# Optimization experiments

Hardware: AMD Instinct MI355X
Metric: run time of the kernel (lower is better)

## Reference

```python
import jax, jax.numpy as jnp
import numpy as np

N, E = 50000, 800000
IN_C, OUT_C, HEADS = 128, 16, 8
EDGE_DIM = 1
NEG_SLOPE = 0.2
LN_EPS = 1e-5


def setup_inputs() -> dict:
    key = jax.random.key(0)
    ks = jax.random.split(key, 12)
    s = 1.0 / np.sqrt(IN_C)
    HC = OUT_C * HEADS
    return {
        "x": jax.random.normal(ks[0], (N, IN_C), jnp.float32),
        "edge_index": jax.random.randint(ks[1], (2, E), 0, N, jnp.int32),
        "edge_attr": jax.random.normal(ks[2], (E, EDGE_DIM), jnp.float32),
        "W": jax.random.normal(ks[3], (IN_C, HC), jnp.float32) * s,
        "b": jnp.zeros((HC,), jnp.float32),
        "att_src": jax.random.normal(ks[4], (HEADS, OUT_C), jnp.float32) * s,
        "att_dst": jax.random.normal(ks[5], (HEADS, OUT_C), jnp.float32) * s,
        "att_edge": jax.random.normal(ks[6], (HEADS, OUT_C), jnp.float32) * s,
        "lin_edge_w": jax.random.normal(ks[7], (EDGE_DIM, HC), jnp.float32) * s,
        "lin_edge_b": jnp.zeros((HC,), jnp.float32),
        "gamma": jnp.ones((HC,), jnp.float32),
        "beta": jnp.zeros((HC,), jnp.float32),
    }


def _segment_softmax(logits, seg, num_segments):
    # numerically-stable softmax over edges grouped by destination node
    m = jax.ops.segment_max(logits, seg, num_segments=num_segments)
    ex = jnp.exp(logits - m[seg])
    z = jax.ops.segment_sum(ex, seg, num_segments=num_segments)
    return ex / (z[seg] + 1e-16)


def reference(x, edge_index, edge_attr, W, b, att_src, att_dst, att_edge,
              lin_edge_w, lin_edge_b, gamma, beta):
    n = x.shape[0]
    src, dst = edge_index[0], edge_index[1]
    # GAT conv: per-head transform, edge-indexed attention, segment softmax, scatter-add
    h = (x @ W).reshape(n, HEADS, OUT_C)                      # [N,H,C]
    a_src = jnp.einsum('nhc,hc->nh', h, att_src)              # [N,H]
    a_dst = jnp.einsum('nhc,hc->nh', h, att_dst)
    e = (edge_attr @ lin_edge_w + lin_edge_b).reshape(-1, HEADS, OUT_C)
    a_edge = jnp.einsum('ehc,hc->eh', e, att_edge)            # [E,H]
    logits = jax.nn.leaky_relu(a_src[src] + a_dst[dst] + a_edge, NEG_SLOPE)
    alpha = _segment_softmax(logits, dst, n)                  # [E,H]
    msg = alpha[..., None] * h[src]                           # [E,H,C]
    out = jax.ops.segment_sum(msg, dst, num_segments=n).reshape(n, -1) + b
    # residual (in_channels == heads*out_channels -> identity projection)
    out = out + x
    # LayerNorm + ELU (dropout is eval-mode identity)
    mu = jnp.mean(out, axis=-1, keepdims=True)
    var = jnp.var(out, axis=-1, keepdims=True)
    out = (out - mu) * jax.lax.rsqrt(var + LN_EPS) * gamma + beta
    return jax.nn.elu(out)
```

## Files before the change

kernel.cpp:

```cpp
#include <hip/hip_runtime.h>
#include <hip/hip_bf16.h>

#define N_NODES 50000
#define N_EDGES 800000
#define IN_C 128
#define HC 128
#define HEADS 8
#define NEG_SLOPE 0.2f
#define LN_EPS 1e-5f

#define LDH 136
#define ELL_CAP 64
#define GEMM_BLOCKS 782
#define FILL_BLOCKS 782
#define FUSED_BLOCKS (GEMM_BLOCKS + FILL_BLOCKS)

typedef __hip_bfloat16 bf16;
typedef __attribute__((ext_vector_type(8))) short short8;
typedef __attribute__((ext_vector_type(4))) float f32x4;

__device__ __forceinline__ float b2f(bf16 v) { return __bfloat162float(v); }

__device__ __forceinline__ unsigned short f2bf(float f) {
    unsigned u = __float_as_uint(f);
    return (unsigned short)((u + 0x7fffu + ((u >> 16) & 1u)) >> 16);
}
__device__ __forceinline__ float bf2f(unsigned s) {
    return __uint_as_float(s << 16);
}
__device__ __forceinline__ short8 pack8(float4 u, float4 v) {
    short8 r;
    r[0] = (short)f2bf(u.x); r[1] = (short)f2bf(u.y);
    r[2] = (short)f2bf(u.z); r[3] = (short)f2bf(u.w);
    r[4] = (short)f2bf(v.x); r[5] = (short)f2bf(v.y);
    r[6] = (short)f2bf(v.z); r[7] = (short)f2bf(v.w);
    return r;
}

__global__ __launch_bounds__(256) void prep(
    const float* __restrict__ W, unsigned short* __restrict__ Wt,
    int* __restrict__ cnt)
{
    int id = blockIdx.x * 256 + threadIdx.x;
    int k = id >> 7, n = id & 127;
    Wt[n * 128 + k] = f2bf(W[id]);
#pragma unroll
    for (int i = 0; i < 4; ++i) {
        int j = id + i * 16384;
        if (j < N_NODES) cnt[j] = 0;
    }
}

__global__ __launch_bounds__(256) void fused(
    const float* __restrict__ x, const unsigned short* __restrict__ Wt,
    const float* __restrict__ att_src, const float* __restrict__ att_dst,
    const int* __restrict__ ei, const float* __restrict__ edge_attr,
    int* __restrict__ cnt, unsigned int* __restrict__ ellp,
    unsigned short* __restrict__ h_out,
    float* __restrict__ a_src, float* __restrict__ a_dst)
{
    __shared__ short sH[4][16 * LDH];
    const int bid = blockIdx.x;
    const int t   = threadIdx.x;

    if (bid & 1) {
        const int fid = bid >> 1;
        const int e0  = (fid * 256 + t) * 4;
        if (e0 >= N_EDGES) return;
        const int4   s4 = *reinterpret_cast<const int4*>(ei + e0);
        const int4   d4 = *reinterpret_cast<const int4*>(ei + N_EDGES + e0);
        const float4 a4 = *reinterpret_cast<const float4*>(edge_attr + e0);

        int p0 = atomicAdd(&cnt[d4.x], 1);
        int p1 = atomicAdd(&cnt[d4.y], 1);
        int p2 = atomicAdd(&cnt[d4.z], 1);
        int p3 = atomicAdd(&cnt[d4.w], 1);
        if (p0 < ELL_CAP)
            ellp[(d4.x << 6) + p0] = (((unsigned)s4.x) << 16) | (unsigned)f2bf(a4.x);
        if (p1 < ELL_CAP)
            ellp[(d4.y << 6) + p1] = (((unsigned)s4.y) << 16) | (unsigned)f2bf(a4.y);
        if (p2 < ELL_CAP)
            ellp[(d4.z << 6) + p2] = (((unsigned)s4.z) << 16) | (unsigned)f2bf(a4.z);
        if (p3 < ELL_CAP)
            ellp[(d4.w << 6) + p3] = (((unsigned)s4.w) << 16) | (unsigned)f2bf(a4.w);
        return;
    }

    const int gid = bid >> 1;
    const int wv  = t >> 6;
    const int l   = t & 63;
    const int gw  = gid * 4 + wv;
    if (gw >= N_NODES / 16) return;

    const int n0   = gw * 16;
    const int mrow = l & 15;
    const int quad = l >> 4;

    short8 afrag[4];
    const float* xr = x + (size_t)(n0 + mrow) * IN_C + quad * 8;
#pragma unroll
    for (int ko = 0; ko < 4; ++ko) {
        float4 u = *reinterpret_cast<const float4*>(xr + ko * 32);
        float4 v = *reinterpret_cast<const float4*>(xr + ko * 32 + 4);
        afrag[ko] = pack8(u, v);
    }

    f32x4 acc[8];
#pragma unroll
    for (int nt = 0; nt < 8; ++nt) acc[nt] = (f32x4)0.f;
#pragma unroll
    for (int nt = 0; nt < 8; ++nt) {
        const unsigned short* wr = Wt + (nt * 16 + mrow) * 128 + quad * 8;
#pragma unroll
        for (int ko = 0; ko < 4; ++ko) {
            short8 bfr = *reinterpret_cast<const short8*>(wr + ko * 32);
            acc[nt] = __builtin_amdgcn_mfma_f32_16x16x32_bf16(afrag[ko], bfr, acc[nt], 0, 0, 0);
        }
    }

#pragma unroll
    for (int nt = 0; nt < 8; ++nt)
#pragma unroll
        for (int r = 0; r < 4; ++r)
            sH[wv][(quad * 4 + r) * LDH + nt * 16 + mrow] = (short)f2bf(acc[nt][r]);

#pragma unroll
    for (int i = 0; i < 4; ++i) {
        int row = i * 4 + (l >> 4);
        int col = (l & 15) * 8;
        short8 hv = *reinterpret_cast<const short8*>(&sH[wv][row * LDH + col]);
        *reinterpret_cast<short8*>(h_out + (size_t)(n0 + row) * HC + col) = hv;
    }

#pragma unroll
    for (int pp = 0; pp < 2; ++pp) {
        int p  = l + pp * 64;
        int m  = p >> 3;
        int hd = p & 7;
        float ssum = 0.f, dsum = 0.f;
#pragma unroll
        for (int c = 0; c < 16; ++c) {
            float hv = bf2f((unsigned short)sH[wv][m * LDH + hd * 16 + c]);
            ssum = fmaf(hv, att_src[hd * 16 + c], ssum);
            dsum = fmaf(hv, att_dst[hd * 16 + c], dsum);
        }
        a_src[(n0 + m) * HEADS + hd] = ssum;
        a_dst[(n0 + m) * HEADS + hd] = dsum;
    }
}

__global__ __launch_bounds__(256) void gather_node(
    const int* __restrict__ cnt, const unsigned int* __restrict__ ellp,
    const float* __restrict__ a_src, const float* __restrict__ a_dst,
    const bf16* __restrict__ h,
    const float* __restrict__ x, const float* __restrict__ bvec,
    const float* __restrict__ gamma, const float* __restrict__ beta,
    const float* __restrict__ att_edge, const float* __restrict__ lin_w,
    const float* __restrict__ lin_b,
    float* __restrict__ out)
{
    const int wave = threadIdx.x >> 6;
    const int l    = threadIdx.x & 63;
    const int n    = blockIdx.x * 4 + wave;
    const int hh   = l >> 3;
    const int jj   = l & 7;

    float ae0 = att_edge[2 * l], ae1 = att_edge[2 * l + 1];
    float p = ae0 * lin_w[2 * l] + ae1 * lin_w[2 * l + 1];
    float q = ae0 * lin_b[2 * l] + ae1 * lin_b[2 * l + 1];
#pragma unroll
    for (int off = 1; off <= 4; off <<= 1) {
        p += __shfl_xor(p, off, 64);
        q += __shfl_xor(q, off, 64);
    }
    const float2 bv = *reinterpret_cast<const float2*>(bvec + 2 * l);
    const float2 gv = *reinterpret_cast<const float2*>(gamma + 2 * l);
    const float2 be = *reinterpret_cast<const float2*>(beta + 2 * l);

    const float ad  = a_dst[n * HEADS + hh];
    const int   beg = n << 6;
    const int   cn  = min(cnt[n], ELL_CAP);
    const int   full = cn & ~7;

    float zp = 0.f, acc0 = 0.f, acc1 = 0.f;
    const __hip_bfloat162* h2 = reinterpret_cast<const __hip_bfloat162*>(h);

    if (full > 0) {
        unsigned ce_c = ellp[beg + jj];
        float    as_c = a_src[(ce_c >> 16) * HEADS + hh];

        for (int bs = 0; bs < full; bs += 8) {
            const unsigned ce = ce_c;
            const float    as = as_c;
            ce_c = ellp[beg + bs + 8 + jj];

            const int   sl = ce >> 16;
            const float ea = bf2f(ce & 0xffffu);
            float lg = as + ad + ea * p + q;
            lg = lg > 0.f ? lg : NEG_SLOPE * lg;
            const float ev = __expf(lg);
            zp += ev;
            const int pk = (sl << 16) | (int)f2bf(ev);

            as_c = a_src[(ce_c >> 16) * HEADS + hh];

#define GSTEP(OFF)                                                        \
            {                                                             \
                int pj = __builtin_amdgcn_ds_swizzle(pk, OFF);            \
                int sj = ((unsigned)pj) >> 16;                            \
                float evj = bf2f((unsigned)pj & 0xffffu);                 \
                __hip_bfloat162 hv = h2[(size_t)sj * 64 + l];             \
                acc0 += evj * b2f(hv.x);                                  \
                acc1 += evj * b2f(hv.y);                                  \
            }
            GSTEP(24)  GSTEP(56)  GSTEP(88)  GSTEP(120)
            GSTEP(152) GSTEP(184) GSTEP(216) GSTEP(248)
#undef GSTEP
        }
    }

    const int rem = cn - full;
    if (rem > 0) {
        int sl = 0; float ev = 0.f;
        if (jj < rem) {
            unsigned ce = ellp[beg + full + jj];
            sl = ce >> 16;
            float ea = bf2f(ce & 0xffffu);
            float lg = a_src[sl * HEADS + hh] + ad + ea * p + q;
            lg = lg > 0.f ? lg : NEG_SLOPE * lg;
            ev = __expf(lg);
        }
        zp += ev;
        const int gbase = l & 56;
        for (int j = 0; j < rem; ++j) {
            float evj = __shfl(ev, gbase | j, 64);
            int   sj  = __shfl(sl, gbase | j, 64);
            __hip_bfloat162 hv = h2[(size_t)sj * 64 + l];
            acc0 += evj * b2f(hv.x);
            acc1 += evj * b2f(hv.y);
        }
    }

    float z = zp;
    z += __shfl_xor(z, 1, 64);
    z += __shfl_xor(z, 2, 64);
    z += __shfl_xor(z, 4, 64);
    const float rz = 1.f / (z + 1e-16f);
    acc0 *= rz;
    acc1 *= rz;

    const size_t idx = (size_t)n * HC + 2 * l;
    const float2 xv = *reinterpret_cast<const float2*>(x + idx);
    float v0 = acc0 + xv.x + bv.x;
    float v1 = acc1 + xv.y + bv.y;
    float s1 = v0 + v1, s2 = v0 * v0 + v1 * v1;
#pragma unroll
    for (int off = 32; off >= 1; off >>= 1) {
        s1 += __shfl_xor(s1, off, 64);
        s2 += __shfl_xor(s2, off, 64);
    }
    const float mean = s1 * (1.f / HC);
    const float var  = s2 * (1.f / HC) - mean * mean;
    const float inv  = rsqrtf(var + LN_EPS);
    float y0 = (v0 - mean) * inv * gv.x + be.x;
    float y1 = (v1 - mean) * inv * gv.y + be.y;
    y0 = y0 > 0.f ? y0 : expm1f(y0);
    y1 = y1 > 0.f ? y1 : expm1f(y1);
    *reinterpret_cast<float2*>(out + idx) = make_float2(y0, y1);
}

extern "C" void kernel_launch(void* const* d_in, const int* in_sizes, int n_in,
                              void* d_out, int out_size, void* d_ws, size_t ws_size,
                              hipStream_t stream)
{
    const float* x         = (const float*)d_in[0];
    const int*   ei        = (const int*)d_in[1];
    const float* edge_attr = (const float*)d_in[2];
    const float* W         = (const float*)d_in[3];
    const float* b         = (const float*)d_in[4];
    const float* att_src   = (const float*)d_in[5];
    const float* att_dst   = (const float*)d_in[6];
    const float* att_edge  = (const float*)d_in[7];
    const float* lin_w     = (const float*)d_in[8];
    const float* lin_b     = (const float*)d_in[9];
    const float* gamma     = (const float*)d_in[10];
    const float* beta      = (const float*)d_in[11];

    char* ws = (char*)d_ws;
    bf16*  h     = (bf16*)ws;  ws += (size_t)N_NODES * HC * sizeof(bf16);
    float* a_src = (float*)ws; ws += (size_t)N_NODES * HEADS * sizeof(float);
    float* a_dst = (float*)ws; ws += (size_t)N_NODES * HEADS * sizeof(float);
    int*   cnt   = (int*)ws;   ws += (size_t)N_NODES * sizeof(int);
    unsigned short* Wt = (unsigned short*)ws;
    ws += (size_t)128 * 128 * sizeof(unsigned short);
    unsigned int* ellp = (unsigned int*)ws;
    ws += (size_t)(N_NODES * ELL_CAP + 64) * sizeof(unsigned int);

    prep<<<64, 256, 0, stream>>>(W, Wt, cnt);

    fused<<<FUSED_BLOCKS, 256, 0, stream>>>(
        x, Wt, att_src, att_dst, ei, edge_attr, cnt, ellp,
        (unsigned short*)h, a_src, a_dst);

    gather_node<<<N_NODES / 4, 256, 0, stream>>>(
        cnt, ellp, a_src, a_dst, h, x, b, gamma, beta,
        att_edge, lin_w, lin_b, (float*)d_out);
}
```

Before: 196.5 us.

## Software-pipeline neighbor row gathers one batch ahead and fold tail into main loop

The gather kernel now prefetches the next batch of eight neighbor h rows into registers while it computes the current batch's softmax weights and FMAs. The separate remainder path is folded into the main loop through masking: out-of-range slots read row 0 and get a zero weight. The weights are also now swizzled as full fp32 instead of packed bf16. ELL fill stores become nontemporal. The aim is to hide gather latency, at the cost of more registers (16 bfloat162 buffers) and possibly lower occupancy.

Result: faster. 188.1 us (-4.3%).

```diff
diff --git a/kernel.cpp b/kernel.cpp
--- a/kernel.cpp
+++ b/kernel.cpp
@@ -75,14 +75,16 @@
         int p1 = atomicAdd(&cnt[d4.y], 1);
         int p2 = atomicAdd(&cnt[d4.z], 1);
         int p3 = atomicAdd(&cnt[d4.w], 1);
-        if (p0 < ELL_CAP)
-            ellp[(d4.x << 6) + p0] = (((unsigned)s4.x) << 16) | (unsigned)f2bf(a4.x);
-        if (p1 < ELL_CAP)
-            ellp[(d4.y << 6) + p1] = (((unsigned)s4.y) << 16) | (unsigned)f2bf(a4.y);
-        if (p2 < ELL_CAP)
-            ellp[(d4.z << 6) + p2] = (((unsigned)s4.z) << 16) | (unsigned)f2bf(a4.z);
-        if (p3 < ELL_CAP)
-            ellp[(d4.w << 6) + p3] = (((unsigned)s4.w) << 16) | (unsigned)f2bf(a4.w);
+#define PUT(P, D, S, A)                                                    \
+        if ((P) < ELL_CAP)                                                 \
+            __builtin_nontemporal_store(                                   \
+                (((unsigned)(S)) << 16) | (unsigned)f2bf(A),               \
+                &ellp[((D) << 6) + (P)]);
+        PUT(p0, d4.x, s4.x, a4.x)
+        PUT(p1, d4.y, s4.y, a4.y)
+        PUT(p2, d4.z, s4.z, a4.z)
+        PUT(p3, d4.w, s4.w, a4.w)
+#undef PUT
         return;
     }
 
@@ -148,6 +150,27 @@
         a_dst[(n0 + m) * HEADS + hd] = dsum;
     }
 }
+
+
+#define LROW(CE, HV, J, OFF, B0)                                           \
+    { int cj_ = __builtin_amdgcn_ds_swizzle((int)(CE), OFF);               \
+      size_t r_ = ((B0) + (J) < cn) ? (size_t)(((unsigned)cj_) >> 16) : 0; \
+      (HV)[J] = h2[r_ * 64 + l]; }
+#define LOADROWS(CE, HV, B0)                                               \
+    LROW(CE, HV, 0,  24, B0) LROW(CE, HV, 1,  56, B0)                      \
+    LROW(CE, HV, 2,  88, B0) LROW(CE, HV, 3, 120, B0)                      \
+    LROW(CE, HV, 4, 152, B0) LROW(CE, HV, 5, 184, B0)                      \
+    LROW(CE, HV, 6, 216, B0) LROW(CE, HV, 7, 248, B0)
+
+#define FROW(EV, HV, J, OFF)                                               \
+    { float evj_ = __uint_as_float((unsigned)__builtin_amdgcn_ds_swizzle(  \
+          __float_as_int(EV), OFF));                                       \
+      acc0 = fmaf(evj_, b2f((HV)[J].x), acc0);                             \
+      acc1 = fmaf(evj_, b2f((HV)[J].y), acc1); }
+#define FMAROWS(EV, HV)                                                    \
+    FROW(EV, HV, 0,  24) FROW(EV, HV, 1,  56) FROW(EV, HV, 2,  88)        \
+    FROW(EV, HV, 3, 120) FROW(EV, HV, 4, 152) FROW(EV, HV, 5, 184)        \
+    FROW(EV, HV, 6, 216) FROW(EV, HV, 7, 248)
 
 __global__ __launch_bounds__(256) void gather_node(
     const int* __restrict__ cnt, const unsigned int* __restrict__ ellp,
@@ -177,67 +200,37 @@
     const float2 gv = *reinterpret_cast<const float2*>(gamma + 2 * l);
     const float2 be = *reinterpret_cast<const float2*>(beta + 2 * l);
 
-    const float ad  = a_dst[n * HEADS + hh];
+    const float adq = a_dst[n * HEADS + hh] + q;
     const int   beg = n << 6;
     const int   cn  = min(cnt[n], ELL_CAP);
-    const int   full = cn & ~7;
 
     float zp = 0.f, acc0 = 0.f, acc1 = 0.f;
     const __hip_bfloat162* h2 = reinterpret_cast<const __hip_bfloat162*>(h);
 
-    if (full > 0) {
+    if (cn > 0) {
         unsigned ce_c = ellp[beg + jj];
         float    as_c = a_src[(ce_c >> 16) * HEADS + hh];
-
-        for (int bs = 0; bs < full; bs += 8) {
-            const unsigned ce = ce_c;
-            const float    as = as_c;
-            ce_c = ellp[beg + bs + 8 + jj];
-
-            const int   sl = ce >> 16;
+        __hip_bfloat162 hv_c[8], hv_n[8];
+        LOADROWS(ce_c, hv_c, 0)
+
+        for (int bs = 0; ; bs += 8) {
+            const unsigned ce   = ce_c;
+            const float    as   = as_c;
+            const bool     last = (bs + 8 >= cn);
+            if (!last) {
+                ce_c = ellp[beg + bs + 8 + jj];
+                LOADROWS(ce_c, hv_n, bs + 8)
+                as_c = a_src[(ce_c >> 16) * HEADS + hh];
+            }
             const float ea = bf2f(ce & 0xffffu);
-            float lg = as + ad + ea * p + q;
-            lg = lg > 0.f ? lg : NEG_SLOPE * lg;
-            const float ev = __expf(lg);
+            float lg = fmaf(ea, p, as + adq);
+            lg = fmaxf(lg, NEG_SLOPE * lg);
+            const float ev = (bs + jj < cn) ? __expf(lg) : 0.f;
             zp += ev;
-            const int pk = (sl << 16) | (int)f2bf(ev);
-
-            as_c = a_src[(ce_c >> 16) * HEADS + hh];
-
-#define GSTEP(OFF)                                                        \
-            {                                                             \
-                int pj = __builtin_amdgcn_ds_swizzle(pk, OFF);            \
-                int sj = ((unsigned)pj) >> 16;                            \
-                float evj = bf2f((unsigned)pj & 0xffffu);                 \
-                __hip_bfloat162 hv = h2[(size_t)sj * 64 + l];             \
-                acc0 += evj * b2f(hv.x);                                  \
-                acc1 += evj * b2f(hv.y);                                  \
-            }
-            GSTEP(24)  GSTEP(56)  GSTEP(88)  GSTEP(120)
-            GSTEP(152) GSTEP(184) GSTEP(216) GSTEP(248)
-#undef GSTEP
-        }
-    }
-
-    const int rem = cn - full;
-    if (rem > 0) {
-        int sl = 0; float ev = 0.f;
-        if (jj < rem) {
-            unsigned ce = ellp[beg + full + jj];
-            sl = ce >> 16;
-            float ea = bf2f(ce & 0xffffu);
-            float lg = a_src[sl * HEADS + hh] + ad + ea * p + q;
-            lg = lg > 0.f ? lg : NEG_SLOPE * lg;
-            ev = __expf(lg);
-        }
-        zp += ev;
-        const int gbase = l & 56;
-        for (int j = 0; j < rem; ++j) {
-            float evj = __shfl(ev, gbase | j, 64);
-            int   sj  = __shfl(sl, gbase | j, 64);
-            __hip_bfloat162 hv = h2[(size_t)sj * 64 + l];
-            acc0 += evj * b2f(hv.x);
-            acc1 += evj * b2f(hv.y);
+            FMAROWS(ev, hv_c)
+            if (last) break;
+#pragma unroll
+            for (int j = 0; j < 8; ++j) hv_c[j] = hv_n[j];
         }
     }
 
```
